# Optimization experiments

Hardware: AMD Instinct MI355X
Metric: run time of the kernel (lower is better)

The kernel has to match this reference:

```python
import jax, jax.numpy as jnp
import numpy as np

B, NOBJ, QD, VD = 128, 36, 2400, 2048
N = B * NOBJ
NEG_SLOPE = 0.2


def _edges():
    # fully connected per image, self-loops included (PyG GATConv adds them)
    base = np.arange(NOBJ)
    src = np.repeat(base, NOBJ)
    dst = np.tile(base, NOBJ)
    off = (np.arange(B) * NOBJ)[:, None]
    return np.stack([(src[None] + off).reshape(-1), (dst[None] + off).reshape(-1)])


def setup_inputs() -> dict:
    key = jax.random.key(0)
    ks = jax.random.split(key, 24)
    p = lambda k, shape, fan: jax.random.normal(k, shape, jnp.float32) * (1.0 / np.sqrt(fan))
    inp = {
        "question_embedding": jax.random.normal(ks[0], (B, QD), jnp.float32),
        "object_features": jax.random.normal(ks[1], (N, VD), jnp.float32),
        "edge_index": jnp.asarray(_edges(), jnp.int32),
        "Wq": p(ks[2], (QD, 2048), QD), "bq": jnp.zeros((2048,), jnp.float32),
        "Wv": p(ks[3], (VD, 2048), VD), "bv": jnp.zeros((2048,), jnp.float32),
        "W1": p(ks[4], (2048, 4 * 256), 2048), "a1s": p(ks[5], (4, 256), 256),
        "a1d": p(ks[6], (4, 256), 256), "b1": jnp.zeros((1024,), jnp.float32),
        "W2": p(ks[7], (1024, 4 * 256), 1024), "a2s": p(ks[8], (4, 256), 256),
        "a2d": p(ks[9], (4, 256), 256), "b2": jnp.zeros((1024,), jnp.float32),
        "W3": p(ks[10], (1024, 5 * 512), 1024), "a3s": p(ks[11], (5, 512), 512),
        "a3d": p(ks[12], (5, 512), 512), "b3": jnp.zeros((512,), jnp.float32),
        "batch_size": B, "num_obj": NOBJ,
    }
    return inp


def gat_conv(x, edge_index, W, a_src, a_dst, b, heads, ch, concat):
    n = x.shape[0]
    h = (x @ W).reshape(n, heads, ch)                       # [N,H,C]
    src, dst = edge_index[0], edge_index[1]
    al_s = jnp.einsum('nhc,hc->nh', h, a_src)               # [N,H]
    al_d = jnp.einsum('nhc,hc->nh', h, a_dst)
    e = jax.nn.leaky_relu(al_s[src] + al_d[dst], NEG_SLOPE)  # [E,H]
    # segment softmax over edges sharing a destination node
    e_max = jax.ops.segment_max(e, dst, num_segments=n)
    e = jnp.exp(e - e_max[dst])
    denom = jax.ops.segment_sum(e, dst, num_segments=n)
    alpha = e / (denom[dst] + 1e-16)                        # [E,H]
    msg = h[src] * alpha[:, :, None]                        # [E,H,C]
    out = jax.ops.segment_sum(msg, dst, num_segments=n)     # [N,H,C]
    out = out.reshape(n, heads * ch) if concat else out.mean(axis=1)
    return out + b


def reference(question_embedding, object_features, edge_index,
              Wq, bq, Wv, bv,
              W1, a1s, a1d, b1,
              W2, a2s, a2d, b2,
              W3, a3s, a3d, b3,
              batch_size, num_obj):
    # hadamard fusion of question with per-object features
    q = question_embedding @ Wq + bq                        # [B,2048]
    q = jnp.repeat(q, num_obj, axis=0)                      # [N,2048]
    v = object_features @ Wv + bv
    x = q * v
    g1 = jax.nn.relu(gat_conv(x, edge_index, W1, a1s, a1d, b1, 4, 256, True))
    g2 = jax.nn.relu(gat_conv(g1, edge_index, W2, a2s, a2d, b2, 4, 256, True))
    g2 = g2 + g1                                            # residual
    return gat_conv(g2, edge_index, W3, a3s, a3d, b3, 5, 512, False)
```

## Files before the change

kernel.cpp:

```cpp
#include <hip/hip_runtime.h>
#include <hip/hip_bf16.h>

typedef unsigned short u16;
typedef __bf16 bf16x8 __attribute__((ext_vector_type(8)));
typedef float f32x4 __attribute__((ext_vector_type(4)));

#define B_IMG 128
#define NOBJ  36
#define NNODE (B_IMG * NOBJ)

__device__ __forceinline__ float b2f(u16 u) {
    union { unsigned int i; float f; } v; v.i = ((unsigned int)u) << 16; return v.f;
}
__device__ __forceinline__ u16 f2b(float f) {
    union { float f; unsigned int i; } v; v.f = f;
    unsigned int u = v.i;
    return (u16)((u + 0x7fffu + ((u >> 16) & 1u)) >> 16);
}

__global__ __launch_bounds__(256)
void conv_mat(const float* __restrict__ src, u16* __restrict__ dst, int n4) {
    const int i = blockIdx.x * 256 + threadIdx.x;
    if (i >= n4) return;
    const float4 f = ((const float4*)src)[i];
    ushort4 o; o.x = f2b(f.x); o.y = f2b(f.y); o.z = f2b(f.z); o.w = f2b(f.w);
    ((ushort4*)dst)[i] = o;
}

__global__ __launch_bounds__(256)
void conv_pad_qe(const float* __restrict__ src, u16* __restrict__ dst) {
    const int i = blockIdx.x * 256 + threadIdx.x;
    if (i >= 128 * 2560) return;
    const int r = i / 2560, c = i - r * 2560;
    dst[i] = (c < 2400) ? f2b(src[r * 2400 + c]) : (u16)0;
}

__global__ __launch_bounds__(256)
void transpose_cvt(const float* __restrict__ src, u16* __restrict__ dst, int R, int C) {
    __shared__ u16 tile[32][33];
    const int bx = blockIdx.x * 32, by = blockIdx.y * 32;
    const int tx = threadIdx.x & 31, ty = threadIdx.x >> 5;
    #pragma unroll
    for (int i = ty; i < 32; i += 8)
        tile[i][tx] = f2b(src[(size_t)(by + i) * C + bx + tx]);
    __syncthreads();
    #pragma unroll
    for (int i = ty; i < 32; i += 8) dst[(size_t)(bx + i) * R + by + tx] = tile[tx][i];
}

__global__ __launch_bounds__(256)
void transpose_cvt_padK(const float* __restrict__ src, u16* __restrict__ dst) {
    __shared__ u16 tile[32][33];
    const int bx = blockIdx.x * 32, by = blockIdx.y * 32;
    const int tx = threadIdx.x & 31, ty = threadIdx.x >> 5;
    #pragma unroll
    for (int i = ty; i < 32; i += 8) {
        const int k = by + i;
        tile[i][tx] = (k < 2400) ? f2b(src[(size_t)k * 2048 + bx + tx]) : (u16)0;
    }
    __syncthreads();
    #pragma unroll
    for (int i = ty; i < 32; i += 8) dst[(size_t)(bx + i) * 2560 + by + tx] = tile[tx][i];
}

template<int EPI>
__global__ __launch_bounds__(256, 4)
void gemm_tn(const u16* __restrict__ A, const u16* __restrict__ Bt,
             int M, int N, int K, int kLen,
             float* __restrict__ Cf, u16* __restrict__ Cb,
             const float* __restrict__ bias, const float* __restrict__ qmul)
{
    __shared__ __align__(16) u16 lds[2 * 8192];

    const int t    = threadIdx.x;
    const int lane = t & 63;
    const int wave = t >> 6;
    const int wr = wave >> 1, wc = wave & 1;
    const int quad = lane >> 4, l16 = lane & 15;
    const int rowBase = blockIdx.y * 128;
    const int colBase = blockIdx.x * 128;
    const int k0 = blockIdx.z * kLen;

    const u16* gA0 = A  + (size_t)(rowBase + wave * 32 + (lane >> 2)) * K + k0 + (lane & 3) * 8;
    const u16* gA1 = gA0 + 16 * (size_t)K;
    const u16* gB0 = Bt + (size_t)(colBase + wave * 32 + (lane >> 2)) * K + k0 + (lane & 3) * 8;
    const u16* gB1 = gB0 + 16 * (size_t)K;
    const int ro = wave * 1024;

    int afr[4], bfr[4];
    #pragma unroll
    for (int r = 0; r < 4; r++) afr[r] = (wr * 64 + r * 16 + l16) * 32 + quad * 8;
    #pragma unroll
    for (int c = 0; c < 4; c++) bfr[c] = 4096 + (wc * 64 + c * 16 + l16) * 32 + quad * 8;

    f32x4 acc[4][4];
    #pragma unroll
    for (int r = 0; r < 4; r++)
        #pragma unroll
        for (int c = 0; c < 4; c++)
            acc[r][c] = (f32x4){0.f, 0.f, 0.f, 0.f};

    auto gld = [](const u16* g, u16* s) {
        __builtin_amdgcn_global_load_lds(
            (const __attribute__((address_space(1))) void*)g,
            (__attribute__((address_space(3))) void*)s, 16, 0, 0);
    };
    auto dma_stage = [&](int it, int st) {
        const int kk = it * 32;
        const int bo = st * 8192;
        gld(gA0 + kk, &lds[bo + ro]);
        gld(gA1 + kk, &lds[bo + ro + 512]);
        gld(gB0 + kk, &lds[bo + 4096 + ro]);
        gld(gB1 + kk, &lds[bo + 4096 + ro + 512]);
    };

    const int nIter = kLen >> 5;
    dma_stage(0, 0);

    for (int it = 0; it < nIter; ++it) {
        asm volatile("s_waitcnt vmcnt(0)\n\ts_barrier" ::: "memory");
        if (it + 1 < nIter) dma_stage(it + 1, (it + 1) & 1);
        const int bo = (it & 1) * 8192;
        bf16x8 avf[4], bvf[4];
        #pragma unroll
        for (int r = 0; r < 4; r++) avf[r] = *(const bf16x8*)&lds[bo + afr[r]];
        #pragma unroll
        for (int c = 0; c < 4; c++) bvf[c] = *(const bf16x8*)&lds[bo + bfr[c]];
        #pragma unroll
        for (int r = 0; r < 4; r++)
            #pragma unroll
            for (int c = 0; c < 4; c++)
                acc[r][c] = __builtin_amdgcn_mfma_f32_16x16x32_bf16(avf[r], bvf[c], acc[r][c], 0, 0, 0);
    }

    #pragma unroll
    for (int r = 0; r < 4; r++) {
        const int mBase = rowBase + wr * 64 + r * 16 + quad * 4;
        #pragma unroll
        for (int c = 0; c < 4; c++) {
            const int n = colBase + wc * 64 + c * 16 + l16;
            #pragma unroll
            for (int e = 0; e < 4; e++) {
                const int m = mBase + e;
                float v = acc[r][c][e];
                if (EPI == 1) {
                    Cf[((size_t)blockIdx.z * M + m) * N + n] = v;
                } else if (EPI == 2) {
                    v += bias[n];
                    v *= qmul[(size_t)(m / NOBJ) * N + n];
                    Cb[(size_t)m * N + n] = f2b(v);
                } else {
                    Cb[(size_t)m * N + n] = f2b(v);
                }
            }
        }
    }
}

__global__ __launch_bounds__(256)
void qcombine(const float* __restrict__ p, const float* __restrict__ bias,
              float* __restrict__ q, int MN, int S)
{
    const int i = blockIdx.x * 256 + threadIdx.x;
    float s = 0.f;
    for (int z = 0; z < S; z++) s += p[(size_t)z * MN + i];
    q[i] = s + bias[i & 2047];
}

template<int H, int C>
__global__ __launch_bounds__(H * 64)
void al_kernel(const u16* __restrict__ h, const float* __restrict__ a_s,
               const float* __restrict__ a_d, float* __restrict__ als, float* __restrict__ ald)
{
    const int n = blockIdx.x;
    const int wv = threadIdx.x >> 6, lane = threadIdx.x & 63;
    constexpr int PL = C / 64;
    const u16*   hp  = h   + (size_t)n * (H * C) + wv * C + lane * PL;
    const float* asp = a_s + wv * C + lane * PL;
    const float* adp = a_d + wv * C + lane * PL;
    u16 hb[PL];
    if constexpr (PL == 4) { *(uint2*)hb = *(const uint2*)hp; }
    else                   { *(uint4*)hb = *(const uint4*)hp; }
    float s1 = 0.f, s2 = 0.f;
    #pragma unroll
    for (int i = 0; i < PL; i++) {
        const float hv = b2f(hb[i]);
        s1 += hv * asp[i];
        s2 += hv * adp[i];
    }
    #pragma unroll
    for (int off = 32; off > 0; off >>= 1) {
        s1 += __shfl_down(s1, off);
        s2 += __shfl_down(s2, off);
    }
    if (lane == 0) { als[n * H + wv] = s1; ald[n * H + wv] = s2; }
}

template<int H, int C, int MODE>
__global__ __launch_bounds__(256)
void attn_kernel(const u16* __restrict__ h, const float* __restrict__ a_src,
                 const float* __restrict__ a_dst, const float* __restrict__ bias,
                 const u16* __restrict__ resid, u16* __restrict__ outb)
{
    __shared__ __align__(16) u16 hl[36 * C];
    __shared__ float alpha[36 * 36];
    __shared__ float asl[36], adl[36];
    __shared__ float psum[36][8][2];
    const int b = blockIdx.y, hd = blockIdx.x;
    const int t = threadIdx.x;
    const int nb = b * NOBJ;
    constexpr int CH = C / 8;
    for (int e = t; e < 36 * CH; e += 256) {
        const int row = e / CH, col = (e - row * CH) * 8;
        *(uint4*)&hl[row * C + col] = *(const uint4*)&h[(size_t)(nb + row) * (H * C) + hd * C + col];
    }
    __syncthreads();
    constexpr int SEG = C / 8;
    for (int e = t; e < 36 * 8; e += 256) {
        const int n = e >> 3, sg = e & 7;
        const u16*   hp = &hl[n * C + sg * SEG];
        const float* as = a_src + hd * C + sg * SEG;
        const float* ad = a_dst + hd * C + sg * SEG;
        float s1 = 0.f, s2 = 0.f;
        #pragma unroll 8
        for (int i = 0; i < SEG; i++) {
            const float hv = b2f(hp[i]);
            s1 += hv * as[i]; s2 += hv * ad[i];
        }
        psum[n][sg][0] = s1; psum[n][sg][1] = s2;
    }
    __syncthreads();
    if (t < 36) {
        float s1 = 0.f, s2 = 0.f;
        #pragma unroll
        for (int sg = 0; sg < 8; sg++) { s1 += psum[t][sg][0]; s2 += psum[t][sg][1]; }
        asl[t] = s1; adl[t] = s2;
    }
    __syncthreads();
    if (t < 36) {
        const float ad = adl[t];
        float mx = -1e30f;
        for (int s = 0; s < 36; s++) {
            float v = asl[s] + ad; v = (v > 0.f) ? v : 0.2f * v;
            alpha[t * 36 + s] = v; mx = fmaxf(mx, v);
        }
        float sum = 0.f;
        for (int s = 0; s < 36; s++) { const float ex = expf(alpha[t * 36 + s] - mx); alpha[t * 36 + s] = ex; sum += ex; }
        const float inv = 1.f / (sum + 1e-16f);
        for (int s = 0; s < 36; s++) alpha[t * 36 + s] *= inv;
    }
    __syncthreads();
    constexpr int NC4 = C / 4;
    for (int e = t; e < 36 * NC4; e += 256) {
        const int d = e / NC4, c4 = (e - d * NC4) * 4;
        float a0 = 0, a1 = 0, a2 = 0, a3 = 0;
        for (int s = 0; s < 36; s++) {
            const float al = alpha[d * 36 + s];
            const ushort4 hv = *(const ushort4*)&hl[s * C + c4];
            a0 += al * b2f(hv.x); a1 += al * b2f(hv.y); a2 += al * b2f(hv.z); a3 += al * b2f(hv.w);
        }
        const int n = nb + d;
        const size_t base = (size_t)n * (H * C) + hd * C + c4;
        const int bb = hd * C + c4;
        float v0 = a0 + bias[bb + 0];
        float v1 = a1 + bias[bb + 1];
        float v2 = a2 + bias[bb + 2];
        float v3 = a3 + bias[bb + 3];
        v0 = v0 > 0.f ? v0 : 0.f; v1 = v1 > 0.f ? v1 : 0.f;
        v2 = v2 > 0.f ? v2 : 0.f; v3 = v3 > 0.f ? v3 : 0.f;
        if (MODE == 2) {
            v0 += b2f(resid[base + 0]); v1 += b2f(resid[base + 1]);
            v2 += b2f(resid[base + 2]); v3 += b2f(resid[base + 3]);
        }
        outb[base + 0] = f2b(v0); outb[base + 1] = f2b(v1);
        outb[base + 2] = f2b(v2); outb[base + 3] = f2b(v3);
    }
}

__global__ __launch_bounds__(256)
void attn_mean_kernel(const u16* __restrict__ h, const float* __restrict__ als,
                      const float* __restrict__ ald, const float* __restrict__ b3,
                      float* __restrict__ outp)
{
    __shared__ __align__(16) u16 hl[36 * 256];
    __shared__ float alpha[36 * 36];
    __shared__ float asl[36], adl[36];
    __shared__ float oacc[36 * 256];
    const int b = blockIdx.y, ch = blockIdx.x;
    const int t = threadIdx.x;
    const int nb = b * NOBJ, cbase = ch * 256;
    for (int e = t; e < 36 * 256; e += 256) oacc[e] = 0.f;
    for (int hd = 0; hd < 5; hd++) {
        __syncthreads();
        if (t < 36) { asl[t] = als[(nb + t) * 5 + hd]; adl[t] = ald[(nb + t) * 5 + hd]; }
        for (int e = t; e < 36 * 32; e += 256) {
            const int row = e >> 5, col = (e & 31) * 8;
            *(uint4*)&hl[row * 256 + col] = *(const uint4*)&h[(size_t)(nb + row) * 2560 + hd * 512 + cbase + col];
        }
        __syncthreads();
        if (t < 36) {
            const float ad = adl[t];
            float mx = -1e30f;
            for (int s = 0; s < 36; s++) {
                float v = asl[s] + ad; v = (v > 0.f) ? v : 0.2f * v;
                alpha[t * 36 + s] = v; mx = fmaxf(mx, v);
            }
            float sum = 0.f;
            for (int s = 0; s < 36; s++) { const float ex = expf(alpha[t * 36 + s] - mx); alpha[t * 36 + s] = ex; sum += ex; }
            const float inv = 1.f / (sum + 1e-16f);
            for (int s = 0; s < 36; s++) alpha[t * 36 + s] *= inv;
        }
        __syncthreads();
        for (int e = t; e < 36 * 64; e += 256) {
            const int d = e >> 6, c4 = (e & 63) * 4;
            float a0 = 0, a1 = 0, a2 = 0, a3 = 0;
            for (int s = 0; s < 36; s++) {
                const float al = alpha[d * 36 + s];
                const ushort4 hv = *(const ushort4*)&hl[s * 256 + c4];
                a0 += al * b2f(hv.x); a1 += al * b2f(hv.y); a2 += al * b2f(hv.z); a3 += al * b2f(hv.w);
            }
            oacc[d * 256 + c4 + 0] += a0; oacc[d * 256 + c4 + 1] += a1;
            oacc[d * 256 + c4 + 2] += a2; oacc[d * 256 + c4 + 3] += a3;
        }
    }
    __syncthreads();
    for (int e = t; e < 36 * 64; e += 256) {
        const int d = e >> 6, c4 = (e & 63) * 4;
        #pragma unroll
        for (int j = 0; j < 4; j++)
            outp[(size_t)(nb + d) * 512 + cbase + c4 + j] =
                oacc[d * 256 + c4 + j] * 0.2f + b3[cbase + c4 + j];
    }
}

extern "C" void kernel_launch(void* const* d_in, const int* in_sizes, int n_in,
                              void* d_out, int out_size, void* d_ws, size_t ws_size,
                              hipStream_t stream)
{
    const float* qe  = (const float*)d_in[0];
    const float* of  = (const float*)d_in[1];
    const float* Wq  = (const float*)d_in[3];
    const float* bq  = (const float*)d_in[4];
    const float* Wv  = (const float*)d_in[5];
    const float* bv  = (const float*)d_in[6];
    const float* W1  = (const float*)d_in[7];
    const float* a1s = (const float*)d_in[8];
    const float* a1d = (const float*)d_in[9];
    const float* b1  = (const float*)d_in[10];
    const float* W2  = (const float*)d_in[11];
    const float* a2s = (const float*)d_in[12];
    const float* a2d = (const float*)d_in[13];
    const float* b2  = (const float*)d_in[14];
    const float* W3  = (const float*)d_in[15];
    const float* a3s = (const float*)d_in[16];
    const float* a3d = (const float*)d_in[17];
    const float* b3  = (const float*)d_in[18];
    float* out = (float*)d_out;
    (void)ws_size; (void)in_sizes; (void)n_in; (void)out_size;

    char* W0 = (char*)d_ws;
    size_t off = 0;
    auto alloc = [&](size_t bytes) -> char* {
        char* p = W0 + off; off += (bytes + 255) & ~(size_t)255; return p;
    };
    u16* qe_c = (u16*)alloc(128ull * 2560 * 2);
    u16* of_c = (u16*)alloc(4608ull * 2048 * 2);
    const size_t szA = 4608ull * 2560 * 2;
    const size_t szB = 4608ull * 1024 * 2;
    const size_t szC = 4608ull * 1024 * 2;
    char* Abase = alloc(szA);
    char* Bbase = alloc(szB);
    char* Cbase = alloc(szC);
    char* Dbase = alloc((size_t)NNODE * 5 * 4 * 2);

    u16*   WqT   = (u16*)Abase;
    float* qpart = (float*)(Abase + 2048ull * 2560 * 2);
    u16*   x     = (u16*)Abase;
    u16*   g1    = (u16*)Abase;
    u16*   h3    = (u16*)Abase;
    u16*   WvT   = (u16*)Bbase;
    float* q     = (float*)(Bbase + 2048ull * 2048 * 2);
    u16*   W1T   = (u16*)Bbase;
    u16*   W2T   = (u16*)Bbase;
    u16*   g2    = (u16*)Bbase;
    u16*   h1    = (u16*)Cbase;
    u16*   h2    = (u16*)Cbase;
    u16*   W3T   = (u16*)Cbase;
    float* als   = (float*)Dbase;
    float* ald   = (float*)(Dbase + (size_t)NNODE * 5 * 4);

    conv_pad_qe<<<(128 * 2560 + 255) / 256, 256, 0, stream>>>(qe, qe_c);
    conv_mat<<<(4608 * 2048 / 4 + 255) / 256, 256, 0, stream>>>(of, of_c, 4608 * 2048 / 4);

    transpose_cvt_padK<<<dim3(64, 80), 256, 0, stream>>>(Wq, WqT);
    gemm_tn<1><<<dim3(16, 1, 5), 256, 0, stream>>>(qe_c, WqT, 128, 2048, 2560, 512,
                                                   qpart, nullptr, nullptr, nullptr);
    qcombine<<<dim3(128 * 2048 / 256), 256, 0, stream>>>(qpart, bq, q, 128 * 2048, 5);

    transpose_cvt<<<dim3(64, 64), 256, 0, stream>>>(Wv, WvT, 2048, 2048);
    gemm_tn<2><<<dim3(16, 36, 1), 256, 0, stream>>>(of_c, WvT, 4608, 2048, 2048, 2048,
                                                    nullptr, x, bv, q);

    transpose_cvt<<<dim3(32, 64), 256, 0, stream>>>(W1, W1T, 2048, 1024);
    gemm_tn<0><<<dim3(8, 36, 1), 256, 0, stream>>>(x, W1T, 4608, 1024, 2048, 2048,
                                                   nullptr, h1, nullptr, nullptr);
    attn_kernel<4, 256, 1><<<dim3(4, B_IMG), 256, 0, stream>>>(h1, a1s, a1d, b1, nullptr, g1);

    transpose_cvt<<<dim3(32, 32), 256, 0, stream>>>(W2, W2T, 1024, 1024);
    gemm_tn<0><<<dim3(8, 36, 1), 256, 0, stream>>>(g1, W2T, 4608, 1024, 1024, 1024,
                                                   nullptr, h2, nullptr, nullptr);
    attn_kernel<4, 256, 2><<<dim3(4, B_IMG), 256, 0, stream>>>(h2, a2s, a2d, b2, g1, g2);

    transpose_cvt<<<dim3(80, 32), 256, 0, stream>>>(W3, W3T, 1024, 2560);
    gemm_tn<0><<<dim3(20, 36, 1), 256, 0, stream>>>(g2, W3T, 4608, 2560, 1024, 1024,
                                                    nullptr, h3, nullptr, nullptr);
    al_kernel<5, 512><<<dim3(NNODE), 320, 0, stream>>>(h3, a3s, a3d, als, ald);
    attn_mean_kernel<<<dim3(2, B_IMG), 256, 0, stream>>>(h3, als, ald, b3, out);
}
```

Measured before the change: 457.3 us.

## Split GAT attention into score, softmax and channel-sliced aggregation kernels

```diff
diff --git a/kernel.cpp b/kernel.cpp
--- a/kernel.cpp
+++ b/kernel.cpp
@@ -196,72 +196,72 @@
     if (lane == 0) { als[n * H + wv] = s1; ald[n * H + wv] = s2; }
 }
 
+template<int H, bool MEAN>
+__global__ __launch_bounds__(64)
+void alpha_kernel(const float* __restrict__ als, const float* __restrict__ ald,
+                  float* __restrict__ alphaG)
+{
+    __shared__ float asl[36];
+    const int b = blockIdx.y, hd = blockIdx.x;
+    const int nb = b * NOBJ;
+    const int t = threadIdx.x;
+    if (t < 36) asl[t] = als[(nb + t) * H + hd];
+    __syncthreads();
+    if (t >= 36) return;
+    const float ad = ald[(nb + t) * H + hd];
+    float row[36];
+    float mx = -1e30f;
+    #pragma unroll
+    for (int s = 0; s < 36; s++) {
+        float v = asl[s] + ad; v = (v > 0.f) ? v : 0.2f * v;
+        row[s] = v; mx = fmaxf(mx, v);
+    }
+    float sum = 0.f;
+    #pragma unroll
+    for (int s = 0; s < 36; s++) { row[s] = expf(row[s] - mx); sum += row[s]; }
+    const float inv = (MEAN ? 0.2f : 1.0f) / (sum + 1e-16f);
+    float* o = alphaG + (((size_t)b * H + hd) * 36 + t) * 36;
+    #pragma unroll
+    for (int s = 0; s < 36; s++) o[s] = row[s] * inv;
+}
+
 template<int H, int C, int MODE>
-__global__ __launch_bounds__(256)
-void attn_kernel(const u16* __restrict__ h, const float* __restrict__ a_src,
-                 const float* __restrict__ a_dst, const float* __restrict__ bias,
-                 const u16* __restrict__ resid, u16* __restrict__ outb)
-{
-    __shared__ __align__(16) u16 hl[36 * C];
-    __shared__ float alpha[36 * 36];
-    __shared__ float asl[36], adl[36];
-    __shared__ float psum[36][8][2];
-    const int b = blockIdx.y, hd = blockIdx.x;
+__global__ __launch_bounds__(192)
+void attn_agg(const u16* __restrict__ h, const float* __restrict__ alphaG,
+              const float* __restrict__ bias, const u16* __restrict__ resid,
+              u16* __restrict__ outb)
+{
+    constexpr int NSLAB = C / 64;
+    __shared__ __align__(16) u16 hl[36 * 64];
+    __shared__ float al[36 * 36];
+    const int b = blockIdx.y;
+    const int hd = blockIdx.x / NSLAB, sl = blockIdx.x - hd * NSLAB;
+    const int nb = b * NOBJ, cb = sl * 64;
     const int t = threadIdx.x;
-    const int nb = b * NOBJ;
-    constexpr int CH = C / 8;
-    for (int e = t; e < 36 * CH; e += 256) {
-        const int row = e / CH, col = (e - row * CH) * 8;
-        *(uint4*)&hl[row * C + col] = *(const uint4*)&h[(size_t)(nb + row) * (H * C) + hd * C + col];
-    }
+
+    for (int e = t; e < 36 * 8; e += 192) {
+        const int row = e >> 3, col = (e & 7) * 8;
+        *(uint4*)&hl[row * 64 + col] =
+            *(const uint4*)&h[(size_t)(nb + row) * (H * C) + hd * C + cb + col];
+    }
+    const float* ap = alphaG + ((size_t)b * H + hd) * 1296;
+    for (int e = t; e < 1296; e += 192) al[e] = ap[e];
     __syncthreads();
-    constexpr int SEG = C / 8;
-    for (int e = t; e < 36 * 8; e += 256) {
-        const int n = e >> 3, sg = e & 7;
-        const u16*   hp = &hl[n * C + sg * SEG];
-        const float* as = a_src + hd * C + sg * SEG;
-        const float* ad = a_dst + hd * C + sg * SEG;
-        float s1 = 0.f, s2 = 0.f;
-        #pragma unroll 8
-        for (int i = 0; i < SEG; i++) {
-            const float hv = b2f(hp[i]);
-            s1 += hv * as[i]; s2 += hv * ad[i];
-        }
-        psum[n][sg][0] = s1; psum[n][sg][1] = s2;
-    }
-    __syncthreads();
-    if (t < 36) {
-        float s1 = 0.f, s2 = 0.f;
-        #pragma unroll
-        for (int sg = 0; sg < 8; sg++) { s1 += psum[t][sg][0]; s2 += psum[t][sg][1]; }
-        asl[t] = s1; adl[t] = s2;
-    }
-    __syncthreads();
-    if (t < 36) {
-        const float ad = adl[t];
-        float mx = -1e30f;
-        for (int s = 0; s < 36; s++) {
-            float v = asl[s] + ad; v = (v > 0.f) ? v : 0.2f * v;
-            alpha[t * 36 + s] = v; mx = fmaxf(mx, v);
-        }
-        float sum = 0.f;
-        for (int s = 0; s < 36; s++) { const float ex = expf(alpha[t * 36 + s] - mx); alpha[t * 36 + s] = ex; sum += ex; }
-        const float inv = 1.f / (sum + 1e-16f);
-        for (int s = 0; s < 36; s++) alpha[t * 36 + s] *= inv;
-    }
-    __syncthreads();
-    constexpr int NC4 = C / 4;
-    for (int e = t; e < 36 * NC4; e += 256) {
-        const int d = e / NC4, c4 = (e - d * NC4) * 4;
+
+    #pragma unroll
+    for (int p = 0; p < 3; p++) {
+        const int e = p * 192 + t;
+        const int d = e >> 4, c4 = (e & 15) * 4;
         float a0 = 0, a1 = 0, a2 = 0, a3 = 0;
         for (int s = 0; s < 36; s++) {
-            const float al = alpha[d * 36 + s];
-            const ushort4 hv = *(const ushort4*)&hl[s * C + c4];
-            a0 += al * b2f(hv.x); a1 += al * b2f(hv.y); a2 += al * b2f(hv.z); a3 += al * b2f(hv.w);
+            const float av = al[d * 36 + s];
+            const ushort4 hv = *(const ushort4*)&hl[s * 64 + c4];
+            a0 += av * b2f(hv.x); a1 += av * b2f(hv.y);
+            a2 += av * b2f(hv.z); a3 += av * b2f(hv.w);
         }
         const int n = nb + d;
-        const size_t base = (size_t)n * (H * C) + hd * C + c4;
-        const int bb = hd * C + c4;
+        const size_t base = (size_t)n * (H * C) + hd * C + cb + c4;
+        const int bb = hd * C + cb + c4;
         float v0 = a0 + bias[bb + 0];
         float v1 = a1 + bias[bb + 1];
         float v2 = a2 + bias[bb + 2];
@@ -277,59 +277,46 @@
     }
 }
 
-__global__ __launch_bounds__(256)
-void attn_mean_kernel(const u16* __restrict__ h, const float* __restrict__ als,
-                      const float* __restrict__ ald, const float* __restrict__ b3,
-                      float* __restrict__ outp)
-{
-    __shared__ __align__(16) u16 hl[36 * 256];
-    __shared__ float alpha[36 * 36];
-    __shared__ float asl[36], adl[36];
-    __shared__ float oacc[36 * 256];
-    const int b = blockIdx.y, ch = blockIdx.x;
+__global__ __launch_bounds__(192)
+void attn_agg_mean(const u16* __restrict__ h, const float* __restrict__ alphaG,
+                   const float* __restrict__ b3, float* __restrict__ outp)
+{
+    __shared__ __align__(16) u16 hl[36 * 64];
+    __shared__ float al[36 * 36];
+    const int b = blockIdx.y, sl = blockIdx.x;
+    const int nb = b * NOBJ, cb = sl * 64;
     const int t = threadIdx.x;
-    const int nb = b * NOBJ, cbase = ch * 256;
-    for (int e = t; e < 36 * 256; e += 256) oacc[e] = 0.f;
+
+    float acc[3][4] = {};
     for (int hd = 0; hd < 5; hd++) {
+        if (hd) __syncthreads();
+        for (int e = t; e < 36 * 8; e += 192) {
+            const int row = e >> 3, col = (e & 7) * 8;
+            *(uint4*)&hl[row * 64 + col] =
+                *(const uint4*)&h[(size_t)(nb + row) * 2560 + hd * 512 + cb + col];
+        }
+        const float* ap = alphaG + ((size_t)b * 5 + hd) * 1296;
+        for (int e = t; e < 1296; e += 192) al[e] = ap[e];
         __syncthreads();
-        if (t < 36) { asl[t] = als[(nb + t) * 5 + hd]; adl[t] = ald[(nb + t) * 5 + hd]; }
-        for (int e = t; e < 36 * 32; e += 256) {
-            const int row = e >> 5, col = (e & 31) * 8;
-            *(uint4*)&hl[row * 256 + col] = *(const uint4*)&h[(size_t)(nb + row) * 2560 + hd * 512 + cbase + col];
+        #pragma unroll
+        for (int p = 0; p < 3; p++) {
+            const int e = p * 192 + t;
+            const int d = e >> 4, c4 = (e & 15) * 4;
+            for (int s = 0; s < 36; s++) {
+                const float av = al[d * 36 + s];
+                const ushort4 hv = *(const ushort4*)&hl[s * 64 + c4];
+                acc[p][0] += av * b2f(hv.x); acc[p][1] += av * b2f(hv.y);
+                acc[p][2] += av * b2f(hv.z); acc[p][3] += av * b2f(hv.w);
+            }
         }
-        __syncthreads();
-        if (t < 36) {
-            const float ad = adl[t];
-            float mx = -1e30f;
-            for (int s = 0; s < 36; s++) {
-                float v = asl[s] + ad; v = (v > 0.f) ? v : 0.2f * v;
-                alpha[t * 36 + s] = v; mx = fmaxf(mx, v);
-            }
-            float sum = 0.f;
-            for (int s = 0; s < 36; s++) { const float ex = expf(alpha[t * 36 + s] - mx); alpha[t * 36 + s] = ex; sum += ex; }
-            const float inv = 1.f / (sum + 1e-16f);
-            for (int s = 0; s < 36; s++) alpha[t * 36 + s] *= inv;
-        }
-        __syncthreads();
-        for (int e = t; e < 36 * 64; e += 256) {
-            const int d = e >> 6, c4 = (e & 63) * 4;
-            float a0 = 0, a1 = 0, a2 = 0, a3 = 0;
-            for (int s = 0; s < 36; s++) {
-                const float al = alpha[d * 36 + s];
-                const ushort4 hv = *(const ushort4*)&hl[s * 256 + c4];
-                a0 += al * b2f(hv.x); a1 += al * b2f(hv.y); a2 += al * b2f(hv.z); a3 += al * b2f(hv.w);
-            }
-            oacc[d * 256 + c4 + 0] += a0; oacc[d * 256 + c4 + 1] += a1;
-            oacc[d * 256 + c4 + 2] += a2; oacc[d * 256 + c4 + 3] += a3;
-        }
-    }
-    __syncthreads();
-    for (int e = t; e < 36 * 64; e += 256) {
-        const int d = e >> 6, c4 = (e & 63) * 4;
+    }
+    #pragma unroll
+    for (int p = 0; p < 3; p++) {
+        const int e = p * 192 + t;
+        const int d = e >> 4, c4 = (e & 15) * 4;
         #pragma unroll
         for (int j = 0; j < 4; j++)
-            outp[(size_t)(nb + d) * 512 + cbase + c4 + j] =
-                oacc[d * 256 + c4 + j] * 0.2f + b3[cbase + c4 + j];
+            outp[(size_t)(nb + d) * 512 + cb + c4 + j] = acc[p][j] + b3[cb + c4 + j];
     }
 }
 
@@ -372,6 +359,7 @@
     char* Bbase = alloc(szB);
     char* Cbase = alloc(szC);
     char* Dbase = alloc((size_t)NNODE * 5 * 4 * 2);
+    float* alphaG = (float*)alloc(128ull * 5 * 36 * 36 * 4);
 
     u16*   WqT   = (u16*)Abase;
     float* qpart = (float*)(Abase + 2048ull * 2560 * 2);
@@ -404,16 +392,21 @@
     transpose_cvt<<<dim3(32, 64), 256, 0, stream>>>(W1, W1T, 2048, 1024);
     gemm_tn<0><<<dim3(8, 36, 1), 256, 0, stream>>>(x, W1T, 4608, 1024, 2048, 2048,
                                                    nullptr, h1, nullptr, nullptr);
-    attn_kernel<4, 256, 1><<<dim3(4, B_IMG), 256, 0, stream>>>(h1, a1s, a1d, b1, nullptr, g1);
+    al_kernel<4, 256><<<dim3(NNODE), 256, 0, stream>>>(h1, a1s, a1d, als, ald);
+    alpha_kernel<4, false><<<dim3(4, B_IMG), 64, 0, stream>>>(als, ald, alphaG);
+    attn_agg<4, 256, 1><<<dim3(16, B_IMG), 192, 0, stream>>>(h1, alphaG, b1, nullptr, g1);
 
     transpose_cvt<<<dim3(32, 32), 256, 0, stream>>>(W2, W2T, 1024, 1024);
     gemm_tn<0><<<dim3(8, 36, 1), 256, 0, stream>>>(g1, W2T, 4608, 1024, 1024, 1024,
                                                    nullptr, h2, nullptr, nullptr);
-    attn_kernel<4, 256, 2><<<dim3(4, B_IMG), 256, 0, stream>>>(h2, a2s, a2d, b2, g1, g2);
+    al_kernel<4, 256><<<dim3(NNODE), 256, 0, stream>>>(h2, a2s, a2d, als, ald);
+    alpha_kernel<4, false><<<dim3(4, B_IMG), 64, 0, stream>>>(als, ald, alphaG);
+    attn_agg<4, 256, 2><<<dim3(16, B_IMG), 192, 0, stream>>>(h2, alphaG, b2, g1, g2);
 
     transpose_cvt<<<dim3(80, 32), 256, 0, stream>>>(W3, W3T, 1024, 2560);
     gemm_tn<0><<<dim3(20, 36, 1), 256, 0, stream>>>(g2, W3T, 4608, 2560, 1024, 1024,
                                                     nullptr, h3, nullptr, nullptr);
     al_kernel<5, 512><<<dim3(NNODE), 320, 0, stream>>>(h3, a3s, a3d, als, ald);
-    attn_mean_kernel<<<dim3(2, B_IMG), 256, 0, stream>>>(h3, als, ald, b3, out);
-}
+    alpha_kernel<5, true><<<dim3(5, B_IMG), 64, 0, stream>>>(als, ald, alphaG);
+    attn_agg_mean<<<dim3(8, B_IMG), 192, 0, stream>>>(h3, alphaG, b3, out);
+}
```

Result: slower. 475.9 us (+4.1%).
